# Optimization experiments

Hardware: AMD Instinct MI355X
Metric: run time of the kernel (lower is better)

## Reference

```python
import jax, jax.numpy as jnp
import numpy as np

WS = 8        # window_size
SHIFT = 4     # shift_size
NH = 6        # num_heads
EPS = 1e-5


def _rel_pos_index(ws):
    coords = np.stack(np.meshgrid(np.arange(ws), np.arange(ws), indexing='ij'))  # [2,ws,ws]
    cf = coords.reshape(2, -1)                      # [2, ws*ws]
    rel = cf[:, :, None] - cf[:, None, :]           # [2, N, N]
    rel = rel.transpose(1, 2, 0)                    # [N, N, 2]
    rel[:, :, 0] += ws - 1
    rel[:, :, 1] += ws - 1
    rel[:, :, 0] *= 2 * ws - 1
    return rel.sum(-1)                              # [N, N] int


def _attn_mask(H, W, ws, shift):
    img = np.zeros((H, W), dtype=np.float32)
    slices = (slice(0, -ws), slice(-ws, -shift), slice(-shift, None))
    cnt = 0
    for hs in slices:
        for wsl in slices:
            img[hs, wsl] = cnt
            cnt += 1
    mw = img.reshape(H // ws, ws, W // ws, ws).transpose(0, 2, 1, 3).reshape(-1, ws * ws)
    diff = mw[:, None, :] - mw[:, :, None]          # [nW, N, N]
    return np.where(diff != 0, -100.0, 0.0).astype(np.float32)


def _layernorm(x, g, b):
    mu = x.mean(-1, keepdims=True)
    var = ((x - mu) ** 2).mean(-1, keepdims=True)
    return (x - mu) * jax.lax.rsqrt(var + EPS) * g + b


def setup_inputs() -> dict:
    key = jax.random.key(0)
    ks = jax.random.split(key, 8)
    C, HID = 192, 768
    return {
        'x': jax.random.normal(ks[0], (8, 128, 128, C), jnp.float32),
        'g1': jnp.ones((C,), jnp.float32),
        'b1': jnp.zeros((C,), jnp.float32),
        'qkv_w': jax.random.normal(ks[1], (3 * C, C), jnp.float32) * 0.02,
        'qkv_b': jnp.zeros((3 * C,), jnp.float32),
        'rpb_table': jax.random.normal(ks[2], ((2 * WS - 1) ** 2, NH), jnp.float32) * 0.02,
        'proj_w': jax.random.normal(ks[3], (C, C), jnp.float32) * 0.02,
        'proj_b': jnp.zeros((C,), jnp.float32),
        'g2': jnp.ones((C,), jnp.float32),
        'b2': jnp.zeros((C,), jnp.float32),
        'fc1_w': jax.random.normal(ks[4], (HID, C), jnp.float32) * 0.02,
        'fc1_b': jnp.zeros((HID,), jnp.float32),
        'fc2_w': jax.random.normal(ks[5], (C, HID), jnp.float32) * 0.02,
        'fc2_b': jnp.zeros((C,), jnp.float32),
    }


def reference(x, g1, b1, qkv_w, qkv_b, rpb_table, proj_w, proj_b, g2, b2,
              fc1_w, fc1_b, fc2_w, fc2_b):
    B, H, W, C = x.shape
    N = WS * WS
    hd = C // NH
    scale = hd ** -0.5

    rpi = jnp.asarray(_rel_pos_index(WS))                 # [N,N] static
    mask = jnp.asarray(_attn_mask(H, W, WS, SHIFT))       # [nW,N,N] static
    nW = mask.shape[0]

    shortcut = x.reshape(B, H * W, C)
    xn = _layernorm(shortcut, g1, b1).reshape(B, H, W, C)

    # cyclic shift
    xs = jnp.roll(xn, shift=(-SHIFT, -SHIFT), axis=(1, 2))

    # window partition -> [B*nW, N, C]
    win = xs.reshape(B, H // WS, WS, W // WS, WS, C).transpose(0, 1, 3, 2, 4, 5)
    win = win.reshape(-1, N, C)
    B_ = win.shape[0]

    # qkv
    qkv = jnp.einsum('bnc,oc->bno', win, qkv_w) + qkv_b   # [B_,N,3C]
    qkv = qkv.reshape(B_, N, 3, NH, hd).transpose(2, 0, 3, 1, 4)  # [3,B_,NH,N,hd]
    q, k, v = qkv[0] * scale, qkv[1], qkv[2]

    attn = jnp.einsum('bhnd,bhmd->bhnm', q, k)            # [B_,NH,N,N]
    bias = rpb_table[rpi.reshape(-1)].reshape(N, N, NH).transpose(2, 0, 1)
    attn = attn + bias[None]
    attn = attn.reshape(B, nW, NH, N, N) + mask[None, :, None]
    attn = jax.nn.softmax(attn.reshape(B_, NH, N, N), axis=-1)

    out = jnp.einsum('bhnm,bhmd->bhnd', attn, v)          # [B_,NH,N,hd]
    out = out.transpose(0, 2, 1, 3).reshape(B_, N, C)
    out = jnp.einsum('bnc,oc->bno', out, proj_w) + proj_b

    # window reverse -> [B,H,W,C]
    out = out.reshape(B, H // WS, W // WS, WS, WS, C).transpose(0, 1, 3, 2, 4, 5)
    out = out.reshape(B, H, W, C)
    out = jnp.roll(out, shift=(SHIFT, SHIFT), axis=(1, 2)).reshape(B, H * W, C)

    x1 = shortcut + out
    h = _layernorm(x1, g2, b2)
    h = jnp.einsum('bnc,hc->bnh', h, fc1_w) + fc1_b
    h = jax.nn.gelu(h, approximate=False)
    h = jnp.einsum('bnh,ch->bnc', h, fc2_w) + fc2_b
    x2 = x1 + h
    return x2.reshape(B, H, W, C)
```

## Files before the change

kernel.cpp:

```cpp
#include <hip/hip_runtime.h>
#include <hip/hip_bf16.h>

typedef __attribute__((ext_vector_type(8))) short s16x8;
typedef __attribute__((ext_vector_type(4))) float f32x4;

__device__ __forceinline__ unsigned short f2bf(float f){
    __hip_bfloat16 h = __float2bfloat16(f);
    return *reinterpret_cast<unsigned short*>(&h);
}

__device__ __forceinline__ int flab(int g){ return (g < 120) ? 0 : ((g < 124) ? 1 : 2); }

__device__ __forceinline__ void async16(const void* g, void* l){
    __builtin_amdgcn_global_load_lds(
        (const __attribute__((address_space(1))) unsigned int*)g,
        (__attribute__((address_space(3))) unsigned int*)l, 16, 0, 0);
}

__global__ __launch_bounds__(256) void wconv_all(
    const float* __restrict__ w0, const float* __restrict__ w1,
    const float* __restrict__ w2, const float* __restrict__ w3,
    unsigned short* __restrict__ o0, unsigned short* __restrict__ o1,
    unsigned short* __restrict__ o2, unsigned short* __restrict__ o3)
{
    int i = blockIdx.x*256 + threadIdx.x;
    if (i < 110592) o0[i] = f2bf(w0[i]);
    if (i < 36864)  o1[i] = f2bf(w1[i]);
    if (i < 147456) o2[i] = f2bf(w2[i]);
    if (i < 147456) o3[i] = f2bf(w3[i]);
}

__global__ __launch_bounds__(256) void lnqkv_kernel(
    const float* __restrict__ x, const float* __restrict__ g1, const float* __restrict__ b1,
    const unsigned short* __restrict__ wq, const float* __restrict__ qkvb,
    unsigned short* __restrict__ qo, unsigned short* __restrict__ ko,
    unsigned short* __restrict__ vo)
{
    __shared__ __attribute__((aligned(16))) unsigned short win[64*200];
    __shared__ __attribute__((aligned(16))) unsigned short Bs[64*200];
    const int b_ = blockIdx.x;
    const int bb = b_>>8, wi = b_&255, wh = wi>>4, ww = wi&15;
    const int tid = threadIdx.x;
    const int wv = tid>>6, lane = tid&63, lrow = lane&15, quad = lane>>4;

    {
        const int n = tid>>2, q4 = tid&3;
        const int r = n>>3, c = n&7;
        const int hh = (wh*8 + r + 4)&127, wp = (ww*8 + c + 4)&127;
        const float* px = x + (((size_t)bb*128+hh)*128+wp)*192 + q4*48;
        float v[48];
        #pragma unroll
        for (int m=0;m<12;++m) *(float4*)(v+m*4) = *(const float4*)(px+m*4);
        float s = 0.f;
        #pragma unroll
        for (int k=0;k<48;++k) s += v[k];
        s += __shfl_xor(s,1); s += __shfl_xor(s,2);
        float mu = s*(1.0f/192.0f);
        float qv = 0.f;
        #pragma unroll
        for (int k=0;k<48;++k){ float d=v[k]-mu; qv += d*d; }
        qv += __shfl_xor(qv,1); qv += __shfl_xor(qv,2);
        float rstd = rsqrtf(qv*(1.0f/192.0f) + 1e-5f);
        const float* pg = g1 + q4*48;
        const float* pb = b1 + q4*48;
        unsigned short* pw = win + n*200 + q4*48;
        #pragma unroll
        for (int k=0;k<48;++k) pw[k] = f2bf((v[k]-mu)*rstd*pg[k] + pb[k]);
    }
    __syncthreads();

    s16x8 af[6];
    #pragma unroll
    for (int kc=0;kc<6;++kc)
        af[kc] = *(const s16x8*)(win + (wv*16+lrow)*200 + kc*32 + quad*8);

    for (int ot=0; ot<9; ++ot) {
        const int o0 = ot*64;
        __syncthreads();
        #pragma unroll
        for (int t=0;t<6;++t) {
            int cid = tid + t*256;
            *(int4*)(Bs + (cid/24)*200 + (cid%24)*8) =
                *(const int4*)(wq + (size_t)o0*192 + cid*8);
        }
        __syncthreads();
        f32x4 acc[4];
        #pragma unroll
        for (int j=0;j<4;++j) acc[j] = (f32x4){0.f,0.f,0.f,0.f};
        #pragma unroll
        for (int kc=0;kc<6;++kc)
            #pragma unroll
            for (int j=0;j<4;++j) {
                s16x8 bf = *(const s16x8*)(Bs + (j*16+lrow)*200 + kc*32 + quad*8);
                acc[j] = __builtin_amdgcn_mfma_f32_16x16x32_bf16(af[kc], bf, acc[j], 0, 0, 0);
            }
        __syncthreads();
        unsigned short* T = Bs;
        const int part = ot/3;
        float bv[4];
        #pragma unroll
        for (int j=0;j<4;++j) bv[j] = qkvb[o0 + j*16 + lrow];

        if (part < 2) {
            const float scale = (part==0) ? 0.17677669529663687f : 1.0f;
            #pragma unroll
            for (int j=0;j<4;++j)
                #pragma unroll
                for (int rg=0;rg<4;++rg) {
                    int n2 = wv*16 + quad*4 + rg;
                    T[n2*72 + j*16 + lrow] = f2bf((acc[j][rg]+bv[j])*scale);
                }
            __syncthreads();
            unsigned short* dst = (part==0) ? qo : ko;
            #pragma unroll
            for (int t=0;t<2;++t) {
                int c = tid + t*256;
                int n2 = c>>3, blk = c&7;
                int o_in = o0 + blk*8 - part*192;
                int head = o_in>>5, d = o_in&31;
                *(int4*)(dst + (((size_t)b_*6+head)*64 + n2)*32 + d) =
                    *(const int4*)(T + n2*72 + blk*8);
            }
        } else {
            #pragma unroll
            for (int j=0;j<4;++j)
                #pragma unroll
                for (int rg=0;rg<4;++rg) {
                    int n2 = wv*16 + quad*4 + rg;
                    T[(j*16+lrow)*72 + n2] = f2bf(acc[j][rg]+bv[j]);
                }
            __syncthreads();
            #pragma unroll
            for (int t=0;t<2;++t) {
                int c = tid + t*256;
                int ol = c>>3, nb = (c&7)*8;
                int o_in = o0 + ol - 384;
                int head = o_in>>5, d = o_in&31;
                *(int4*)(vo + (((size_t)b_*6+head)*32 + d)*64 + nb) =
                    *(const int4*)(T + ol*72 + nb);
            }
        }
    }
}

__global__ __launch_bounds__(384) void attn_kernel(
    const unsigned short* __restrict__ q, const unsigned short* __restrict__ k,
    const unsigned short* __restrict__ vT, const float* __restrict__ rpb,
    unsigned short* __restrict__ ao)
{
    __shared__ float rpb_s[1350];
    __shared__ __attribute__((aligned(16))) unsigned short p_lds[6*4608];
    const int b_ = blockIdx.x;
    const int h = threadIdx.x >> 6;
    const int lane = threadIdx.x & 63, lrow = lane & 15, quad = lane >> 4;
    for (int i = threadIdx.x; i < 1350; i += 384) rpb_s[i] = rpb[i];
    __syncthreads();

    const size_t hb = ((size_t)b_*6 + h)*2048;
    const unsigned short* qb = q  + hb;
    const unsigned short* kb = k  + hb;
    const unsigned short* vb = vT + hb;

    s16x8 qf[4], kf[4];
    #pragma unroll
    for (int i = 0; i < 4; ++i) qf[i] = *(const s16x8*)(qb + (i*16+lrow)*32 + quad*8);
    #pragma unroll
    for (int j = 0; j < 4; ++j) kf[j] = *(const s16x8*)(kb + (j*16+lrow)*32 + quad*8);

    const f32x4 zz = {0.f,0.f,0.f,0.f};
    f32x4 s[4][4];
    #pragma unroll
    for (int i = 0; i < 4; ++i)
        #pragma unroll
        for (int j = 0; j < 4; ++j)
            s[i][j] = __builtin_amdgcn_mfma_f32_16x16x32_bf16(qf[i], kf[j], zz, 0, 0, 0);

    const int wi = b_ & 255, wh = wi >> 4, ww = wi & 15;
    int labm[4];
    #pragma unroll
    for (int j = 0; j < 4; ++j) {
        int m = j*16 + lrow;
        labm[j] = flab(wh*8 + (m >> 3))*3 + flab(ww*8 + (m & 7));
    }
    unsigned short* pl = p_lds + h*4608;
    #pragma unroll
    for (int i = 0; i < 4; ++i) {
        #pragma unroll
        for (int rg = 0; rg < 4; ++rg) {
            int n = i*16 + quad*4 + rg;
            int rn = n >> 3, cn = n & 7;
            int labn = flab(wh*8 + rn)*3 + flab(ww*8 + cn);
            float vals[4];
            float vmax = -1e30f;
            #pragma unroll
            for (int j = 0; j < 4; ++j) {
                int m = j*16 + lrow;
                int idx = ((rn - (m >> 3) + 7)*15 + (cn - (m & 7) + 7))*6 + h;
                float val = s[i][j][rg] + rpb_s[idx];
                if (labn != labm[j]) val -= 100.f;
                vals[j] = val;
                vmax = fmaxf(vmax, val);
            }
            #pragma unroll
            for (int o = 1; o < 16; o <<= 1) vmax = fmaxf(vmax, __shfl_xor(vmax, o));
            float sum = 0.f;
            #pragma unroll
            for (int j = 0; j < 4; ++j) { vals[j] = __expf(vals[j] - vmax); sum += vals[j]; }
            #pragma unroll
            for (int o = 1; o < 16; o <<= 1) sum += __shfl_xor(sum, o);
            float inv = 1.f / sum;
            #pragma unroll
            for (int j = 0; j < 4; ++j) pl[n*72 + j*16 + lrow] = f2bf(vals[j]*inv);
        }
    }
    __syncthreads();

    f32x4 oacc[4][2];
    #pragma unroll
    for (int i = 0; i < 4; ++i) { oacc[i][0] = zz; oacc[i][1] = zz; }
    #pragma unroll
    for (int kc = 0; kc < 2; ++kc) {
        s16x8 vf[2];
        #pragma unroll
        for (int jd = 0; jd < 2; ++jd)
            vf[jd] = *(const s16x8*)(vb + (jd*16+lrow)*64 + kc*32 + quad*8);
        #pragma unroll
        for (int i = 0; i < 4; ++i) {
            s16x8 pf = *(const s16x8*)(pl + (i*16+lrow)*72 + kc*32 + quad*8);
            #pragma unroll
            for (int jd = 0; jd < 2; ++jd)
                oacc[i][jd] = __builtin_amdgcn_mfma_f32_16x16x32_bf16(pf, vf[jd], oacc[i][jd], 0, 0, 0);
        }
    }
    unsigned short* ob = ao + (size_t)b_*12288 + h*32;
    #pragma unroll
    for (int i = 0; i < 4; ++i)
        #pragma unroll
        for (int jd = 0; jd < 2; ++jd)
            #pragma unroll
            for (int rg = 0; rg < 4; ++rg) {
                int n = i*16 + quad*4 + rg;
                ob[(size_t)n*192 + jd*16 + lrow] = f2bf(oacc[i][jd][rg]);
            }
}

__global__ __launch_bounds__(256) void projln_kernel(
    const unsigned short* __restrict__ A, const unsigned short* __restrict__ W,
    const float* __restrict__ pbias, const float* __restrict__ x,
    const float* __restrict__ g2, const float* __restrict__ b2,
    float* __restrict__ x1, unsigned short* __restrict__ xln2)
{
    __shared__ __attribute__((aligned(16))) char smem[36864];
    unsigned short* As = (unsigned short*)smem;
    unsigned short* Bs = (unsigned short*)(smem + 9216);
    const int b_ = blockIdx.x;
    const int tid = threadIdx.x, wv = tid>>6, lane = tid&63;
    const int lrow = lane&15, quad = lane>>4;
    const size_t m0 = (size_t)b_*64;

    f32x4 acc[12];
    #pragma unroll
    for (int j=0;j<12;++j) acc[j] = (f32x4){0.f,0.f,0.f,0.f};

    for (int k0=0;k0<192;k0+=64) {
        __syncthreads();
        #pragma unroll
        for (int t=0;t<2;++t) {
            int cid = tid + t*256;
            *(int4*)(As + (cid>>3)*72 + (cid&7)*8) =
                *(const int4*)(A + (m0 + (cid>>3))*192 + k0 + (cid&7)*8);
        }
        #pragma unroll
        for (int t=0;t<6;++t) {
            int cid = tid + t*256;
            *(int4*)(Bs + (cid>>3)*72 + (cid&7)*8) =
                *(const int4*)(W + (size_t)(cid>>3)*192 + k0 + (cid&7)*8);
        }
        __syncthreads();
        #pragma unroll
        for (int kc=0;kc<2;++kc) {
            s16x8 af = *(const s16x8*)(As + (wv*16+lrow)*72 + kc*32 + quad*8);
            #pragma unroll
            for (int j=0;j<12;++j) {
                s16x8 bf = *(const s16x8*)(Bs + (j*16+lrow)*72 + kc*32 + quad*8);
                acc[j] = __builtin_amdgcn_mfma_f32_16x16x32_bf16(af, bf, acc[j], 0, 0, 0);
            }
        }
    }
    __syncthreads();

    const int bb = b_>>8, wi = b_&255, wh = wi>>4, ww = wi&15;
    float bv[12], gv[12], b2v[12];
    #pragma unroll
    for (int j=0;j<12;++j) {
        bv[j]  = pbias[j*16+lrow];
        gv[j]  = g2[j*16+lrow];
        b2v[j] = b2[j*16+lrow];
    }
    unsigned short* T = (unsigned short*)smem;
    #pragma unroll
    for (int rg=0;rg<4;++rg) {
        int n2 = wv*16 + quad*4 + rg;
        int r = n2>>3, c = n2&7;
        int hh = (wh*8+r+4)&127, wp = (ww*8+c+4)&127;
        size_t tok = ((size_t)bb*128+hh)*128 + wp;
        float xv[12];
        float s = 0.f;
        #pragma unroll
        for (int j=0;j<12;++j) {
            float t = acc[j][rg] + bv[j] + x[tok*192 + j*16 + lrow];
            xv[j] = t; s += t;
        }
        #pragma unroll
        for (int o=1;o<16;o<<=1) s += __shfl_xor(s, o);
        float mu = s*(1.0f/192.0f);
        float qv = 0.f;
        #pragma unroll
        for (int j=0;j<12;++j){ float d = xv[j]-mu; qv += d*d; }
        #pragma unroll
        for (int o=1;o<16;o<<=1) qv += __shfl_xor(qv, o);
        float rstd = rsqrtf(qv*(1.0f/192.0f) + 1e-5f);
        #pragma unroll
        for (int j=0;j<12;++j) {
            x1[tok*192 + j*16 + lrow] = xv[j];
            T[n2*200 + j*16 + lrow] = f2bf((xv[j]-mu)*rstd*gv[j] + b2v[j]);
        }
    }
    __syncthreads();
    #pragma unroll
    for (int t=0;t<6;++t) {
        int cid = tid + t*256;
        int n2 = cid/24, blk = cid%24;
        int r = n2>>3, c = n2&7;
        int hh = (wh*8+r+4)&127, wp = (ww*8+c+4)&127;
        size_t tok = ((size_t)bb*128+hh)*128 + wp;
        *(int4*)(xln2 + tok*192 + blk*8) = *(const int4*)(T + n2*200 + blk*8);
    }
}

__device__ __forceinline__ void mm128x96(
    const unsigned short* __restrict__ A, const unsigned short* __restrict__ W,
    int K, size_t m0, int o0, unsigned short* As, unsigned short* Bs,
    f32x4 (&acc)[2][6])
{
    const int tid = threadIdx.x, wv = tid>>6, lane = tid&63;
    const int lrow = lane&15, quad = lane>>4;
    const int lr4 = lane>>2, lc4 = lane&3;
    const int cb = lc4 ^ (lr4&3);
    #pragma unroll
    for (int i=0;i<2;++i)
        #pragma unroll
        for (int j=0;j<6;++j) acc[i][j] = (f32x4){0.f,0.f,0.f,0.f};

    const unsigned short* Abase = A + (m0 + lr4)*(size_t)K + cb*8;
    const unsigned short* Wbase = W + ((size_t)(o0 + lr4))*K + cb*8;

    #pragma unroll
    for (int it=0;it<2;++it) {
        int ia = wv + it*4;
        async16(Abase + (size_t)(ia*16)*K, As + ia*512);
    }
    #pragma unroll
    for (int it=0;it<2;++it) {
        int ib = wv + it*4;
        if (ib < 6) async16(Wbase + (size_t)(ib*16)*K, Bs + ib*512);
    }

    int cur = 0;
    for (int k0=0; k0<K; k0+=32) {
        __syncthreads();
        if (k0 + 32 < K) {
            unsigned short* An = As + (cur^1)*4096;
            unsigned short* Bn = Bs + (cur^1)*3072;
            #pragma unroll
            for (int it=0;it<2;++it) {
                int ia = wv + it*4;
                async16(Abase + (size_t)(ia*16)*K + (k0+32), An + ia*512);
            }
            #pragma unroll
            for (int it=0;it<2;++it) {
                int ib = wv + it*4;
                if (ib < 6) async16(Wbase + (size_t)(ib*16)*K + (k0+32), Bn + ib*512);
            }
        }
        const unsigned short* Ac = As + cur*4096;
        const unsigned short* Bc = Bs + cur*3072;
        const int rs = (quad ^ (lrow&3)) << 3;
        s16x8 af[2], bf[6];
        #pragma unroll
        for (int i=0;i<2;++i)
            af[i] = *(const s16x8*)(Ac + (wv*32 + i*16 + lrow)*32 + rs);
        #pragma unroll
        for (int j=0;j<6;++j)
            bf[j] = *(const s16x8*)(Bc + (j*16 + lrow)*32 + rs);
        #pragma unroll
        for (int i=0;i<2;++i)
            #pragma unroll
            for (int j=0;j<6;++j)
                acc[i][j] = __builtin_amdgcn_mfma_f32_16x16x32_bf16(af[i], bf[j], acc[i][j], 0, 0, 0);
        cur ^= 1;
    }
}

__global__ __launch_bounds__(256, 4) void gemm_fc1_kernel(
    const unsigned short* __restrict__ A, const unsigned short* __restrict__ Wm,
    const float* __restrict__ bias, unsigned short* __restrict__ h1)
{
    __shared__ __attribute__((aligned(16))) char smem[28672];
    unsigned short* As = (unsigned short*)smem;
    unsigned short* Bs = (unsigned short*)(smem + 16384);
    const int bid = blockIdx.x;
    const int virt = (bid & 7)*1024 + (bid >> 3);
    const size_t m0 = (size_t)(virt >> 3)*128;
    const int o0 = (virt & 7)*96;
    f32x4 acc[2][6];
    mm128x96(A, Wm, 192, m0, o0, As, Bs, acc);
    const int tid = threadIdx.x, wv = tid>>6, lane = tid&63;
    const int lrow = lane&15, quad = lane>>4;
    float bv[6];
    #pragma unroll
    for (int j=0;j<6;++j) bv[j] = bias[o0 + j*16 + lrow];
    __syncthreads();
    unsigned short* T = (unsigned short*)smem;
    #pragma unroll
    for (int i=0;i<2;++i)
        #pragma unroll
        for (int j=0;j<6;++j)
            #pragma unroll
            for (int rg=0;rg<4;++rg) {
                int ml = wv*32 + i*16 + quad*4 + rg;
                float v = acc[i][j][rg] + bv[j];
                float v2 = v*v;
                float z = v*(1.5957691216057308f + 0.07135481627f*v2);
                float r = v * __builtin_amdgcn_rcpf(1.f + __expf(-z));
                T[ml*104 + j*16 + lrow] = f2bf(r);
            }
    __syncthreads();
    #pragma unroll
    for (int t=0;t<6;++t) {
        int c = tid + t*256;
        int row = c/12, blk = c%12;
        *(int4*)(h1 + (m0+row)*768 + o0 + blk*8) = *(const int4*)(T + row*104 + blk*8);
    }
}

__global__ __launch_bounds__(256, 4) void gemm_fc2_kernel(
    const unsigned short* __restrict__ A, const unsigned short* __restrict__ Wm,
    const float* __restrict__ bias, const float* __restrict__ x1, float* __restrict__ out)
{
    __shared__ __attribute__((aligned(16))) char smem[28672];
    unsigned short* As = (unsigned short*)smem;
    unsigned short* Bs = (unsigned short*)(smem + 16384);
    const int bid = blockIdx.x;
    const int virt = (bid & 7)*256 + (bid >> 3);
    const size_t m0 = (size_t)(virt >> 1)*128;
    const int o0 = (virt & 1)*96;
    f32x4 acc[2][6];
    mm128x96(A, Wm, 768, m0, o0, As, Bs, acc);
    const int tid = threadIdx.x, wv = tid>>6, lane = tid&63;
    const int lrow = lane&15, quad = lane>>4;
    float bv[6];
    #pragma unroll
    for (int j=0;j<6;++j) bv[j] = bias[o0 + j*16 + lrow];
    float* T = (float*)smem;
    #pragma unroll
    for (int p=0;p<2;++p) {
        __syncthreads();
        if ((wv>>1) == p) {
            int wl = wv&1;
            #pragma unroll
            for (int i=0;i<2;++i)
                #pragma unroll
                for (int j=0;j<6;++j)
                    #pragma unroll
                    for (int rg=0;rg<4;++rg)
                        T[(wl*32 + i*16 + quad*4 + rg)*100 + j*16 + lrow] = acc[i][j][rg] + bv[j];
        }
        __syncthreads();
        #pragma unroll
        for (int t=0;t<6;++t) {
            int c = tid + t*256;
            int row = c/24, blk = c%24;
            size_t ad = (m0 + p*64 + row)*192 + o0 + blk*4;
            float4 v = *(const float4*)(T + row*100 + blk*4);
            float4 rx = *(const float4*)(x1 + ad);
            v.x += rx.x; v.y += rx.y; v.z += rx.z; v.w += rx.w;
            *(float4*)(out + ad) = v;
        }
    }
}

extern "C" void kernel_launch(void* const* d_in, const int* in_sizes, int n_in,
                              void* d_out, int out_size, void* d_ws, size_t ws_size,
                              hipStream_t stream)
{
    const float* x      = (const float*)d_in[0];
    const float* g1     = (const float*)d_in[1];
    const float* b1     = (const float*)d_in[2];
    const float* qkv_w  = (const float*)d_in[3];
    const float* qkv_b  = (const float*)d_in[4];
    const float* rpb    = (const float*)d_in[5];
    const float* proj_w = (const float*)d_in[6];
    const float* proj_b = (const float*)d_in[7];
    const float* g2     = (const float*)d_in[8];
    const float* b2     = (const float*)d_in[9];
    const float* fc1_w  = (const float*)d_in[10];
    const float* fc1_b  = (const float*)d_in[11];
    const float* fc2_w  = (const float*)d_in[12];
    const float* fc2_b  = (const float*)d_in[13];
    float* out = (float*)d_out;
    char* ws = (char*)d_ws;

    if (ws_size < 353206272ULL) return;

    unsigned short* qbuf  = (unsigned short*)(ws + 0);
    unsigned short* kbuf  = (unsigned short*)(ws + 50331648);
    unsigned short* vbuf  = (unsigned short*)(ws + 100663296);
    unsigned short* attnO = (unsigned short*)(ws + 150994944);
    float*          x1    = (float*)        (ws + 201326592);
    unsigned short* xln2  = (unsigned short*)(ws + 301989888);
    unsigned short* wq    = (unsigned short*)(ws + 352321536);
    unsigned short* wp    = (unsigned short*)(ws + 352321536 + 221184);
    unsigned short* w1    = (unsigned short*)(ws + 352321536 + 221184 + 73728);
    unsigned short* w2    = (unsigned short*)(ws + 352321536 + 221184 + 73728 + 294912);
    unsigned short* h1    = (unsigned short*)(ws + 0);

    wconv_all<<<576, 256, 0, stream>>>(qkv_w, proj_w, fc1_w, fc2_w, wq, wp, w1, w2);
    lnqkv_kernel<<<2048, 256, 0, stream>>>(x, g1, b1, wq, qkv_b, qbuf, kbuf, vbuf);
    attn_kernel<<<2048, 384, 0, stream>>>(qbuf, kbuf, vbuf, rpb, attnO);
    projln_kernel<<<2048, 256, 0, stream>>>(attnO, wp, proj_b, x, g2, b2, x1, xln2);
    gemm_fc1_kernel<<<8192, 256, 0, stream>>>(xln2, w1, fc1_b, h1);
    gemm_fc2_kernel<<<2048, 256, 0, stream>>>(h1, w2, fc2_b, x1, out);
}
```

Before: 566.5 us.

## Triple-buffer MLP GEMM loads with explicit vmcnt waits and new LDS swizzle

The shared 128x96 GEMM mainloop moves from double buffering with a full __syncthreads per k-step to a three-stage ring of async global-to-LDS loads. Explicit s_waitcnt vmcnt counts plus raw s_barrier let two tiles stay in flight while the current one is consumed. K becomes a template parameter so the loop can be fully specialised, and the LDS XOR swizzle is changed to a row-pair pattern. LDS per block grows from 28 KB to 42 KB and launch bounds drop from 4 to 3 blocks per CU, so occupancy is traded for deeper prefetch.

```diff
diff --git a/kernel.cpp b/kernel.cpp
--- a/kernel.cpp
+++ b/kernel.cpp
@@ -338,54 +338,37 @@
     }
 }
 
+template<int K>
 __device__ __forceinline__ void mm128x96(
     const unsigned short* __restrict__ A, const unsigned short* __restrict__ W,
-    int K, size_t m0, int o0, unsigned short* As, unsigned short* Bs,
+    size_t m0, int o0, unsigned short* As, unsigned short* Bs,
     f32x4 (&acc)[2][6])
 {
     const int tid = threadIdx.x, wv = tid>>6, lane = tid&63;
     const int lrow = lane&15, quad = lane>>4;
-    const int lr4 = lane>>2, lc4 = lane&3;
-    const int cb = lc4 ^ (lr4&3);
+    const int grow = lane>>2;
+    const int gcb  = (lane&3) ^ ((lane>>3)&3);
     #pragma unroll
     for (int i=0;i<2;++i)
         #pragma unroll
         for (int j=0;j<6;++j) acc[i][j] = (f32x4){0.f,0.f,0.f,0.f};
 
-    const unsigned short* Abase = A + (m0 + lr4)*(size_t)K + cb*8;
-    const unsigned short* Wbase = W + ((size_t)(o0 + lr4))*K + cb*8;
-
-    #pragma unroll
-    for (int it=0;it<2;++it) {
-        int ia = wv + it*4;
-        async16(Abase + (size_t)(ia*16)*K, As + ia*512);
-    }
-    #pragma unroll
-    for (int it=0;it<2;++it) {
-        int ib = wv + it*4;
-        if (ib < 6) async16(Wbase + (size_t)(ib*16)*K, Bs + ib*512);
-    }
-
-    int cur = 0;
-    for (int k0=0; k0<K; k0+=32) {
-        __syncthreads();
-        if (k0 + 32 < K) {
-            unsigned short* An = As + (cur^1)*4096;
-            unsigned short* Bn = Bs + (cur^1)*3072;
-            #pragma unroll
-            for (int it=0;it<2;++it) {
-                int ia = wv + it*4;
-                async16(Abase + (size_t)(ia*16)*K + (k0+32), An + ia*512);
-            }
-            #pragma unroll
-            for (int it=0;it<2;++it) {
-                int ib = wv + it*4;
-                if (ib < 6) async16(Wbase + (size_t)(ib*16)*K + (k0+32), Bn + ib*512);
-            }
-        }
-        const unsigned short* Ac = As + cur*4096;
-        const unsigned short* Bc = Bs + cur*3072;
-        const int rs = (quad ^ (lrow&3)) << 3;
+    const unsigned short* Ab = A + (m0 + grow)*(size_t)K + gcb*8;
+    const unsigned short* Wb = W + ((size_t)(o0 + grow))*K + gcb*8;
+
+    auto issue = [&](int k0, int buf) {
+        unsigned short* Ad = As + buf*4096;
+        unsigned short* Bd = Bs + buf*3072;
+        async16(Ab + (size_t)(wv*16)*K + k0,     Ad + wv*512);
+        async16(Ab + (size_t)((wv+4)*16)*K + k0, Ad + (wv+4)*512);
+        async16(Wb + (size_t)(wv*16)*K + k0,     Bd + wv*512);
+        if (wv < 2)
+            async16(Wb + (size_t)((wv+4)*16)*K + k0, Bd + (wv+4)*512);
+    };
+    auto compute = [&](int buf) {
+        const unsigned short* Ac = As + buf*4096;
+        const unsigned short* Bc = Bs + buf*3072;
+        const int rs = (quad ^ ((lrow>>1)&3)) << 3;
         s16x8 af[2], bf[6];
         #pragma unroll
         for (int i=0;i<2;++i)
@@ -398,23 +381,48 @@
             #pragma unroll
             for (int j=0;j<6;++j)
                 acc[i][j] = __builtin_amdgcn_mfma_f32_16x16x32_bf16(af[i], bf[j], acc[i][j], 0, 0, 0);
-        cur ^= 1;
-    }
-}
-
-__global__ __launch_bounds__(256, 4) void gemm_fc1_kernel(
+    };
+
+    constexpr int NT = K/32;
+    issue(0, 0);
+    issue(32, 1);
+    int cur = 0;
+    for (int t = 0; t < NT-2; ++t) {
+        if (wv < 2) asm volatile("s_waitcnt vmcnt(4)" ::: "memory");
+        else        asm volatile("s_waitcnt vmcnt(3)" ::: "memory");
+        __builtin_amdgcn_s_barrier();
+        asm volatile("" ::: "memory");
+        int nb = cur + 2; if (nb >= 3) nb -= 3;
+        issue((t+2)*32, nb);
+        asm volatile("" ::: "memory");
+        compute(cur);
+        cur = (cur == 2) ? 0 : cur + 1;
+    }
+    if (wv < 2) asm volatile("s_waitcnt vmcnt(4)" ::: "memory");
+    else        asm volatile("s_waitcnt vmcnt(3)" ::: "memory");
+    __builtin_amdgcn_s_barrier();
+    asm volatile("" ::: "memory");
+    compute(cur);
+    cur = (cur == 2) ? 0 : cur + 1;
+    asm volatile("s_waitcnt vmcnt(0)" ::: "memory");
+    __builtin_amdgcn_s_barrier();
+    asm volatile("" ::: "memory");
+    compute(cur);
+}
+
+__global__ __launch_bounds__(256, 3) void gemm_fc1_kernel(
     const unsigned short* __restrict__ A, const unsigned short* __restrict__ Wm,
     const float* __restrict__ bias, unsigned short* __restrict__ h1)
 {
-    __shared__ __attribute__((aligned(16))) char smem[28672];
+    __shared__ __attribute__((aligned(16))) char smem[43008];
     unsigned short* As = (unsigned short*)smem;
-    unsigned short* Bs = (unsigned short*)(smem + 16384);
+    unsigned short* Bs = (unsigned short*)(smem + 24576);
     const int bid = blockIdx.x;
     const int virt = (bid & 7)*1024 + (bid >> 3);
     const size_t m0 = (size_t)(virt >> 3)*128;
     const int o0 = (virt & 7)*96;
     f32x4 acc[2][6];
-    mm128x96(A, Wm, 192, m0, o0, As, Bs, acc);
+    mm128x96<192>(A, Wm, m0, o0, As, Bs, acc);
     const int tid = threadIdx.x, wv = tid>>6, lane = tid&63;
     const int lrow = lane&15, quad = lane>>4;
     float bv[6];
@@ -444,19 +452,19 @@
     }
 }
 
-__global__ __launch_bounds__(256, 4) void gemm_fc2_kernel(
+__global__ __launch_bounds__(256, 3) void gemm_fc2_kernel(
     const unsigned short* __restrict__ A, const unsigned short* __restrict__ Wm,
     const float* __restrict__ bias, const float* __restrict__ x1, float* __restrict__ out)
 {
-    __shared__ __attribute__((aligned(16))) char smem[28672];
+    __shared__ __attribute__((aligned(16))) char smem[43008];
     unsigned short* As = (unsigned short*)smem;
-    unsigned short* Bs = (unsigned short*)(smem + 16384);
+    unsigned short* Bs = (unsigned short*)(smem + 24576);
     const int bid = blockIdx.x;
     const int virt = (bid & 7)*256 + (bid >> 3);
     const size_t m0 = (size_t)(virt >> 1)*128;
     const int o0 = (virt & 1)*96;
     f32x4 acc[2][6];
-    mm128x96(A, Wm, 768, m0, o0, As, Bs, acc);
+    mm128x96<768>(A, Wm, m0, o0, As, Bs, acc);
     const int tid = threadIdx.x, wv = tid>>6, lane = tid&63;
     const int lrow = lane&15, quad = lane>>4;
     float bv[6];
```

Measured after the change: 579.4 us. +2.3%, slower.
